# Performance work log

Hardware: AMD Instinct MI355X
Metric: run time of the kernel (lower is better)

Reference implementation:

```python
import jax, jax.numpy as jnp
import numpy as np

B, N, D = 2, 8192, 3


def setup_inputs() -> dict:
    key = jax.random.key(0)
    k1, k2, k3 = jax.random.split(key, 3)
    pc1 = jax.random.normal(k1, (B, N, D), dtype=jnp.float32)
    pc2 = jax.random.normal(k2, (B, N, D), dtype=jnp.float32)
    flow = jax.random.normal(k3, (B, N, D), dtype=jnp.float32) * 0.1
    return {"pc1": pc1, "pc2": pc2, "flow": flow}


def reference(pc1, pc2, flow):
    loss_norm = 2
    a = pc1 + flow  # warped pc1, (B, N, 3)
    # pairwise squared distances (B, N, M); argmin of d2 == argmin of true dist
    d2 = (
        jnp.sum(a * a, axis=-1)[:, :, None]
        + jnp.sum(pc2 * pc2, axis=-1)[:, None, :]
        - 2.0 * jnp.einsum("bnd,bmd->bnm", a, pc2)
    )
    # 1-NN of each warped pc1 point in pc2 (idx detached: argmin is non-diff)
    idx1 = jnp.argmin(d2, axis=2)  # (B, N)
    nn1 = jnp.take_along_axis(pc2, idx1[..., None], axis=1)  # (B, N, 3)
    diff1 = a - nn1
    dist1 = jnp.sum(jnp.abs(diff1) ** loss_norm, axis=-1) ** (1.0 / loss_norm)
    # 1-NN of each pc2 point in warped pc1
    idx2 = jnp.argmin(d2, axis=1)  # (B, M)
    nn2 = jnp.take_along_axis(a, idx2[..., None], axis=1)  # (B, M, 3)
    diff2 = pc2 - nn2
    dist2 = jnp.sum(jnp.abs(diff2) ** loss_norm, axis=-1) ** (1.0 / loss_norm)
    return jnp.mean(dist1 + dist2)
```

## Files before the change

### kernel.cpp

```cpp
#include <hip/hip_runtime.h>
#include <math.h>

#define N_PTS   8192
#define BATCH   2
#define NTHR    256
#define QPT     2
#define QPB     (NTHR * QPT)
#define NQB     (N_PTS / QPB)
#define NCHUNK  16
#define CHUNKC  (N_PTS / NCHUNK)
#define TOTQ    (BATCH * 2 * N_PTS)


__global__ __launch_bounds__(256) void chamfer_prep(const float* __restrict__ pc1,
                                                    const float* __restrict__ pc2,
                                                    const float* __restrict__ flow,
                                                    float4* __restrict__ cand,
                                                    float* __restrict__ accum) {
    int i = blockIdx.x * 256 + threadIdx.x;
    if (i < BATCH * N_PTS) {
        float px = pc2[i * 3 + 0], py = pc2[i * 3 + 1], pz = pc2[i * 3 + 2];
        cand[i] = make_float4(-2.f * px, -2.f * py, -2.f * pz,
                              px * px + py * py + pz * pz);
        float wx = pc1[i * 3 + 0] + flow[i * 3 + 0];
        float wy = pc1[i * 3 + 1] + flow[i * 3 + 1];
        float wz = pc1[i * 3 + 2] + flow[i * 3 + 2];
        cand[BATCH * N_PTS + i] = make_float4(-2.f * wx, -2.f * wy, -2.f * wz,
                                              wx * wx + wy * wy + wz * wz);
    }
    if (i == 0) *accum = 0.0f;
}

__global__ __launch_bounds__(NTHR) void chamfer_nn(const float4* __restrict__ cand,
                                                   float* __restrict__ res) {
    const int qb    = blockIdx.x % NQB;
    const int chunk = blockIdx.x / NQB;
    const int b     = blockIdx.y;
    const int dir   = blockIdx.z;

    const float4* __restrict__ qarr =
        cand + ((size_t)(1 - dir) * BATCH + b) * N_PTS;
    const float4* __restrict__ db =
        cand + ((size_t)dir * BATCH + b) * N_PTS + (size_t)chunk * CHUNKC;

    const int q0 = qb * QPB + threadIdx.x;
    const int q1 = q0 + NTHR;

    float4 c0 = qarr[q0];
    float4 c1 = qarr[q1];
    const float qx0 = -0.5f * c0.x, qy0 = -0.5f * c0.y, qz0 = -0.5f * c0.z;
    const float qx1 = -0.5f * c1.x, qy1 = -0.5f * c1.y, qz1 = -0.5f * c1.z;
    const float q2_0 = c0.w, q2_1 = c1.w;

    float m0 = 3.402823466e38f, m1 = 3.402823466e38f;

    #pragma unroll 8
    for (int j = 0; j < CHUNKC; ++j) {
        float4 c = db[j];
        float t0 = fmaf(qz0, c.z, c.w);
        t0 = fmaf(qy0, c.y, t0);
        t0 = fmaf(qx0, c.x, t0);
        m0 = fminf(m0, t0);
        float t1 = fmaf(qz1, c.z, c.w);
        t1 = fmaf(qy1, c.y, t1);
        t1 = fmaf(qx1, c.x, t1);
        m1 = fminf(m1, t1);
    }

    const size_t slot = ((size_t)dir * BATCH + b) * N_PTS;
    res[(size_t)chunk * TOTQ + slot + q0] = m0 + q2_0;
    res[(size_t)chunk * TOTQ + slot + q1] = m1 + q2_1;
}

__global__ __launch_bounds__(256) void chamfer_reduce(const float* __restrict__ res,
                                                      float* __restrict__ accum) {
    const int i = blockIdx.x * 256 + threadIdx.x;
    float m = res[i];
    #pragma unroll
    for (int c = 1; c < NCHUNK; ++c)
        m = fminf(m, res[(size_t)c * TOTQ + i]);
    float v = sqrtf(fmaxf(m, 0.0f));

    for (int off = 32; off > 0; off >>= 1)
        v += __shfl_down(v, off, 64);

    __shared__ float wsum[4];
    const int wave = threadIdx.x >> 6;
    if ((threadIdx.x & 63) == 0) wsum[wave] = v;
    __syncthreads();
    if (threadIdx.x == 0)
        atomicAdd(accum, wsum[0] + wsum[1] + wsum[2] + wsum[3]);
}

__global__ void chamfer_finalize(const float* __restrict__ accum,
                                 float* __restrict__ out) {
    out[0] = accum[0] * (1.0f / (float)(BATCH * N_PTS));
}

extern "C" void kernel_launch(void* const* d_in, const int* in_sizes, int n_in,
                              void* d_out, int out_size, void* d_ws, size_t ws_size,
                              hipStream_t stream) {
    const float* pc1  = (const float*)d_in[0];
    const float* pc2  = (const float*)d_in[1];
    const float* flow = (const float*)d_in[2];
    float* out = (float*)d_out;

    float4* cand = (float4*)d_ws;
    float*  res  = (float*)(cand + 2 * BATCH * N_PTS);
    float*  accum = res + (size_t)NCHUNK * TOTQ;

    chamfer_prep<<<(BATCH * N_PTS + 255) / 256, 256, 0, stream>>>(pc1, pc2, flow, cand, accum);

    dim3 grid(NQB * NCHUNK, BATCH, 2);
    chamfer_nn<<<grid, NTHR, 0, stream>>>(cand, res);

    chamfer_reduce<<<TOTQ / 256, 256, 0, stream>>>(res, accum);
    chamfer_finalize<<<1, 1, 0, stream>>>(accum, out);
}
```

Baseline: 52.45 us.

## Merge chunk partial minima with atomicMin and fold finalize into reduce

Instead of writing a per-chunk partial-min array and reducing it later, each NN block does an atomicMin on the non-negative float bit pattern, so only one min buffer exists. Queries per thread go from 2 to 4 and the chunk count from 16 to 32, which raises register reuse of each loaded candidate. The separate finalize kernel is removed by having the last reduce block, found with an atomic counter, write the mean. This saves one launch and the traffic of the partial buffer, at the cost of atomic contention and possibly lower occupancy.

Result: faster. 46.22 us (-11.9%).

```diff
diff --git a/kernel.cpp b/kernel.cpp
--- a/kernel.cpp
+++ b/kernel.cpp
@@ -4,20 +4,24 @@
 #define N_PTS   8192
 #define BATCH   2
 #define NTHR    256
-#define QPT     2
+#define QPT     4
 #define QPB     (NTHR * QPT)
 #define NQB     (N_PTS / QPB)
-#define NCHUNK  16
+#define NCHUNK  32
 #define CHUNKC  (N_PTS / NCHUNK)
 #define TOTQ    (BATCH * 2 * N_PTS)
+#define RBLK    (TOTQ / 256)
 
 
 __global__ __launch_bounds__(256) void chamfer_prep(const float* __restrict__ pc1,
                                                     const float* __restrict__ pc2,
                                                     const float* __restrict__ flow,
                                                     float4* __restrict__ cand,
-                                                    float* __restrict__ accum) {
+                                                    unsigned int* __restrict__ minbits,
+                                                    float* __restrict__ accum,
+                                                    unsigned int* __restrict__ counter) {
     int i = blockIdx.x * 256 + threadIdx.x;
+    minbits[i] = 0x7F7FFFFFu;
     if (i < BATCH * N_PTS) {
         float px = pc2[i * 3 + 0], py = pc2[i * 3 + 1], pz = pc2[i * 3 + 2];
         cand[i] = make_float4(-2.f * px, -2.f * py, -2.f * pz,
@@ -28,11 +32,11 @@
         cand[BATCH * N_PTS + i] = make_float4(-2.f * wx, -2.f * wy, -2.f * wz,
                                               wx * wx + wy * wy + wz * wz);
     }
-    if (i == 0) *accum = 0.0f;
+    if (i == 0) { *accum = 0.0f; *counter = 0u; }
 }
 
 __global__ __launch_bounds__(NTHR) void chamfer_nn(const float4* __restrict__ cand,
-                                                   float* __restrict__ res) {
+                                                   unsigned int* __restrict__ minbits) {
     const int qb    = blockIdx.x % NQB;
     const int chunk = blockIdx.x / NQB;
     const int b     = blockIdx.y;
@@ -44,42 +48,45 @@
         cand + ((size_t)dir * BATCH + b) * N_PTS + (size_t)chunk * CHUNKC;
 
     const int q0 = qb * QPB + threadIdx.x;
-    const int q1 = q0 + NTHR;
 
-    float4 c0 = qarr[q0];
-    float4 c1 = qarr[q1];
-    const float qx0 = -0.5f * c0.x, qy0 = -0.5f * c0.y, qz0 = -0.5f * c0.z;
-    const float qx1 = -0.5f * c1.x, qy1 = -0.5f * c1.y, qz1 = -0.5f * c1.z;
-    const float q2_0 = c0.w, q2_1 = c1.w;
-
-    float m0 = 3.402823466e38f, m1 = 3.402823466e38f;
+    float qx[QPT], qy[QPT], qz[QPT], q2[QPT], m[QPT];
+    #pragma unroll
+    for (int k = 0; k < QPT; ++k) {
+        float4 c = qarr[q0 + k * NTHR];
+        qx[k] = -0.5f * c.x;
+        qy[k] = -0.5f * c.y;
+        qz[k] = -0.5f * c.z;
+        q2[k] = c.w;
+        m[k]  = 3.402823466e38f;
+    }
 
     #pragma unroll 8
     for (int j = 0; j < CHUNKC; ++j) {
         float4 c = db[j];
-        float t0 = fmaf(qz0, c.z, c.w);
-        t0 = fmaf(qy0, c.y, t0);
-        t0 = fmaf(qx0, c.x, t0);
-        m0 = fminf(m0, t0);
-        float t1 = fmaf(qz1, c.z, c.w);
-        t1 = fmaf(qy1, c.y, t1);
-        t1 = fmaf(qx1, c.x, t1);
-        m1 = fminf(m1, t1);
+        #pragma unroll
+        for (int k = 0; k < QPT; ++k) {
+            float t = fmaf(qz[k], c.z, c.w);
+            t = fmaf(qy[k], c.y, t);
+            t = fmaf(qx[k], c.x, t);
+            m[k] = fminf(m[k], t);
+        }
     }
 
-    const size_t slot = ((size_t)dir * BATCH + b) * N_PTS;
-    res[(size_t)chunk * TOTQ + slot + q0] = m0 + q2_0;
-    res[(size_t)chunk * TOTQ + slot + q1] = m1 + q2_1;
+    unsigned int* __restrict__ slot =
+        minbits + ((size_t)dir * BATCH + b) * N_PTS;
+    #pragma unroll
+    for (int k = 0; k < QPT; ++k) {
+        float d2 = fmaxf(m[k] + q2[k], 0.0f);
+        atomicMin(&slot[q0 + k * NTHR], __float_as_uint(d2));
+    }
 }
 
-__global__ __launch_bounds__(256) void chamfer_reduce(const float* __restrict__ res,
-                                                      float* __restrict__ accum) {
+__global__ __launch_bounds__(256) void chamfer_reduce(const unsigned int* __restrict__ minbits,
+                                                      float* __restrict__ accum,
+                                                      unsigned int* __restrict__ counter,
+                                                      float* __restrict__ out) {
     const int i = blockIdx.x * 256 + threadIdx.x;
-    float m = res[i];
-    #pragma unroll
-    for (int c = 1; c < NCHUNK; ++c)
-        m = fminf(m, res[(size_t)c * TOTQ + i]);
-    float v = sqrtf(fmaxf(m, 0.0f));
+    float v = sqrtf(__uint_as_float(minbits[i]));
 
     for (int off = 32; off > 0; off >>= 1)
         v += __shfl_down(v, off, 64);
@@ -88,13 +95,15 @@
     const int wave = threadIdx.x >> 6;
     if ((threadIdx.x & 63) == 0) wsum[wave] = v;
     __syncthreads();
-    if (threadIdx.x == 0)
+    if (threadIdx.x == 0) {
         atomicAdd(accum, wsum[0] + wsum[1] + wsum[2] + wsum[3]);
-}
-
-__global__ void chamfer_finalize(const float* __restrict__ accum,
-                                 float* __restrict__ out) {
-    out[0] = accum[0] * (1.0f / (float)(BATCH * N_PTS));
+        __threadfence();
+        unsigned int old = atomicAdd(counter, 1u);
+        if (old == RBLK - 1) {
+            float total = atomicAdd(accum, 0.0f);
+            out[0] = total * (1.0f / (float)(BATCH * N_PTS));
+        }
+    }
 }
 
 extern "C" void kernel_launch(void* const* d_in, const int* in_sizes, int n_in,
@@ -106,14 +115,15 @@
     float* out = (float*)d_out;
 
     float4* cand = (float4*)d_ws;
-    float*  res  = (float*)(cand + 2 * BATCH * N_PTS);
-    float*  accum = res + (size_t)NCHUNK * TOTQ;
+    unsigned int* minbits = (unsigned int*)(cand + 2 * BATCH * N_PTS);
+    float* accum = (float*)(minbits + TOTQ);
+    unsigned int* counter = (unsigned int*)(accum + 1);
 
-    chamfer_prep<<<(BATCH * N_PTS + 255) / 256, 256, 0, stream>>>(pc1, pc2, flow, cand, accum);
+    chamfer_prep<<<TOTQ / 256, 256, 0, stream>>>(pc1, pc2, flow, cand, minbits,
+                                                 accum, counter);
 
     dim3 grid(NQB * NCHUNK, BATCH, 2);
-    chamfer_nn<<<grid, NTHR, 0, stream>>>(cand, res);
+    chamfer_nn<<<grid, NTHR, 0, stream>>>(cand, minbits);
 
-    chamfer_reduce<<<TOTQ / 256, 256, 0, stream>>>(res, accum);
-    chamfer_finalize<<<1, 1, 0, stream>>>(accum, out);
+    chamfer_reduce<<<RBLK, 256, 0, stream>>>(minbits, accum, counter, out);
 }
```
